# Performance work log

Hardware: AMD Instinct MI355X
Metric: run time of the kernel (lower is better)

Reference implementation:

```python
import jax, jax.numpy as jnp
import numpy as np

N_HEADS = 8
D_K = 64
NEG = 1e9


def setup_inputs() -> dict:
    key = jax.random.key(0)
    k1, k2, k3 = jax.random.split(key, 3)
    B, L, C = 4, 2048, 512
    x = jax.random.normal(k1, (B, L, C), dtype=jnp.float32)
    W_in = jax.random.normal(k2, (C, N_HEADS * D_K * 3), dtype=jnp.float32) * (C ** -0.5)
    b_in = jnp.zeros((N_HEADS * D_K * 3,), dtype=jnp.float32)
    W_out = jax.random.normal(k3, (N_HEADS * D_K, C), dtype=jnp.float32) * ((N_HEADS * D_K) ** -0.5)
    b_out = jnp.zeros((C,), dtype=jnp.float32)
    return {"x": x, "W_in": W_in, "b_in": b_in, "W_out": W_out, "b_out": b_out}


def reference(x, W_in, b_in, W_out, b_out):
    B, L, C = x.shape
    H, Dk = N_HEADS, D_K
    scale = Dk ** -0.5
    qkv = x @ W_in + b_in                       # [B, L, 3*H*Dk]
    qkv = qkv.reshape(B, L, H, 3 * Dk)
    q, k, v = jnp.split(qkv, 3, axis=-1)         # each [B, L, H, Dk]
    attn = jnp.einsum('bihd,bjhd->bijh', q, k) * scale  # [B, L, L, H]
    mask = jnp.tril(jnp.ones((L, L), dtype=x.dtype))[None, :, :, None]
    attn = attn * mask - NEG * (1.0 - mask)
    attn = jax.nn.softmax(attn, axis=2)          # softmax over j
    res = jnp.einsum('bijh,bjhd->bihd', attn, v)  # [B, L, H, Dk]
    res = res.reshape(B, L, H * Dk)
    res = res @ W_out + b_out
    return res + x
```

## Files before the change

### kernel.cpp

```cpp
#include <hip/hip_runtime.h>
#include <math.h>
#include <cstddef>


constexpr int B_SZ  = 4;
constexpr int L_SEQ = 2048;
constexpr int C_DIM = 512;
constexpr int H_N   = 8;
constexpr int DK    = 64;
constexpr int N_QKV = 1536;
constexpr int M_ROWS = B_SZ * L_SEQ;
constexpr float SCALE = 0.125f;
constexpr float DEFER_THR = 8.f;

typedef __attribute__((ext_vector_type(4))) float f32x4;
typedef __attribute__((ext_vector_type(8))) short bf16x8;

static __device__ inline ushort f2bf(float f) {
  unsigned u = __builtin_bit_cast(unsigned, f);
  u += 0x7fffu + ((u >> 16) & 1u);
  return (ushort)(u >> 16);
}

typedef __attribute__((address_space(1))) const unsigned int* gas1_t;
typedef __attribute__((address_space(3))) unsigned int* las3_t;
static __device__ inline void gload_lds16(const void* g, void* l) {
  __builtin_amdgcn_global_load_lds((gas1_t)g, (las3_t)l, 16, 0, 0);
}


__global__ __launch_bounds__(256) void convert_bf16(
    const float* __restrict__ src, ushort* __restrict__ dst, int n4) {
  const int i = blockIdx.x * 256 + threadIdx.x;
  if (i < n4) {
    const float4 v = reinterpret_cast<const float4*>(src)[i];
    ushort4 o;
    o.x = f2bf(v.x); o.y = f2bf(v.y); o.z = f2bf(v.z); o.w = f2bf(v.w);
    reinterpret_cast<ushort4*>(dst)[i] = o;
  }
}

__global__ __launch_bounds__(256) void transpose_bf16(
    const float* __restrict__ src, ushort* __restrict__ dst, int R, int C) {
  __shared__ ushort T[64][65];
  const int c0 = blockIdx.x * 64, r0 = blockIdx.y * 64;
#pragma unroll
  for (int p = 0; p < 16; ++p) {
    const int idx = threadIdx.x + p * 256;
    const int r = idx >> 6, c = idx & 63;
    T[r][c] = f2bf(src[(size_t)(r0 + r) * C + c0 + c]);
  }
  __syncthreads();
#pragma unroll
  for (int p = 0; p < 16; ++p) {
    const int idx = threadIdx.x + p * 256;
    const int r = idx >> 6, c = idx & 63;
    dst[(size_t)(c0 + r) * R + r0 + c] = T[c][r];
  }
}

template <int EPI>
__global__ __launch_bounds__(256) void gemm_bf16(
    const ushort* __restrict__ A, const ushort* __restrict__ Bt,
    const float* __restrict__ bias, ushort* __restrict__ Qo,
    ushort* __restrict__ Ko, ushort* __restrict__ Vto,
    float* __restrict__ outF, const float* __restrict__ resid,
    int N, int K) {
  __shared__ ushort Al[128 * 32];
  __shared__ ushort Bl[128 * 32];
  const int tid = threadIdx.x;
  const int w = tid >> 6, l = tid & 63;
  const int cc = l & 15, gg = l >> 4;
  const int bm = blockIdx.y * 128, bn = blockIdx.x * 128;
  const int wr = w >> 1, wc = w & 1;
  f32x4 acc[4][4] = {};

  for (int k0 = 0; k0 < K; k0 += 32) {
#pragma unroll
    for (int q = 0; q < 2; ++q) {
      const int cbase = q * 256 + w * 64;
      const int c = cbase + l;
      gload_lds16(A + (size_t)(bm + (c >> 2)) * K + k0 + (c & 3) * 8,
                  &Al[cbase * 8]);
      gload_lds16(Bt + (size_t)(bn + (c >> 2)) * K + k0 + (c & 3) * 8,
                  &Bl[cbase * 8]);
    }
    __syncthreads();
    bf16x8 aF[4], bF[4];
#pragma unroll
    for (int i = 0; i < 4; ++i)
      aF[i] = *reinterpret_cast<const bf16x8*>(
          &Al[(wr * 64 + i * 16 + cc) * 32 + gg * 8]);
#pragma unroll
    for (int j = 0; j < 4; ++j)
      bF[j] = *reinterpret_cast<const bf16x8*>(
          &Bl[(wc * 64 + j * 16 + cc) * 32 + gg * 8]);
#pragma unroll
    for (int i = 0; i < 4; ++i)
#pragma unroll
      for (int j = 0; j < 4; ++j)
        acc[i][j] = __builtin_amdgcn_mfma_f32_16x16x32_bf16(aF[i], bF[j],
                                                            acc[i][j], 0, 0, 0);
    __syncthreads();
  }

  if (EPI == 0) {
#pragma unroll
    for (int j = 0; j < 4; ++j) {
      const int colbase = bn + wc * 64 + j * 16;
      const int h = colbase / 192, rem = colbase % 192;
      const int type = rem / 64, d = (rem % 64) + cc;
      const float bv = bias[colbase + cc];
#pragma unroll
      for (int i = 0; i < 4; ++i) {
        const int rowbase = bm + wr * 64 + i * 16 + 4 * gg;
        const int b = rowbase >> 11, ll = rowbase & 2047;
        const size_t bh32 = (size_t)(b * H_N + h) * 32;
        if (type == 0) {
#pragma unroll
          for (int r = 0; r < 4; ++r)
            Qo[((size_t)(b * H_N + h) * L_SEQ + ll + r) * DK + d] =
                f2bf(acc[i][j][r] + bv);
        } else if (type == 1) {
#pragma unroll
          for (int r = 0; r < 4; ++r) {
            const int jg = ll + r;
            Ko[(bh32 + (jg >> 6)) * 4096 + (jg & 63) * 64 +
               (((d >> 3) ^ (jg & 7)) << 3) + (d & 7)] =
                f2bf(acc[i][j][r] + bv);
          }
        } else {
          ushort4 pk;
          pk.x = f2bf(acc[i][j][0] + bv);
          pk.y = f2bf(acc[i][j][1] + bv);
          pk.z = f2bf(acc[i][j][2] + bv);
          pk.w = f2bf(acc[i][j][3] + bv);
          const size_t idx = (bh32 + (ll >> 6)) * 4096 + (size_t)d * 64 +
                             ((((ll & 63) >> 3) ^ (d & 7)) << 3) + (ll & 7);
          *reinterpret_cast<ushort4*>(&Vto[idx]) = pk;
        }
      }
    }
  } else {
#pragma unroll
    for (int j = 0; j < 4; ++j) {
      const int col = bn + wc * 64 + j * 16 + cc;
      const float bv = bias[col];
#pragma unroll
      for (int i = 0; i < 4; ++i) {
        const int rowbase = bm + wr * 64 + i * 16 + 4 * gg;
#pragma unroll
        for (int r = 0; r < 4; ++r) {
          const size_t off = (size_t)(rowbase + r) * N + col;
          outF[off] = acc[i][j][r] + bv + resid[off];
        }
      }
    }
  }
}

#define STAGE(buf, tile)                                                     \
  {                                                                          \
    const ushort* kg_ = KoB + (size_t)(tile) * 4096 + w * 1024 + lane * 8;   \
    const ushort* vg_ = VtB + (size_t)(tile) * 4096 + w * 1024 + lane * 8;   \
    gload_lds16(kg_, &Ks[buf][w * 1024]);                                    \
    gload_lds16(kg_ + 512, &Ks[buf][w * 1024 + 512]);                        \
    gload_lds16(vg_, &Vs[buf][w * 1024]);                                    \
    gload_lds16(vg_ + 512, &Vs[buf][w * 1024 + 512]);                        \
  }

__global__ __launch_bounds__(256, 4) void attn_mfma(
    const ushort* __restrict__ Q, const ushort* __restrict__ Ko,
    const ushort* __restrict__ Vt, ushort* __restrict__ attn_out) {
  __shared__ ushort Ks[2][4096];
  __shared__ ushort Vs[2][4096];
  __shared__ ushort Pw_s[4][1024];
  const int id = blockIdx.x;
  const int bh = (id & 7) + 8 * ((id >> 3) & 3);
  const int qt = 31 - (id >> 5);
  const int tid = threadIdx.x;
  const int w = tid >> 6, lane = tid & 63;
  const int c = lane & 15, g = lane >> 4;
  const int b = bh >> 3, h = bh & 7;
  const ushort* KoB = Ko + (size_t)bh * 32 * 4096;
  const ushort* VtB = Vt + (size_t)bh * 32 * 4096;
  const int q0 = qt * 64 + w * 16;
  ushort* Pw = Pw_s[w];
  const int pc0 = (g ^ (c & 7)) * 8;
  const int pc1 = ((g + 4) ^ (c & 7)) * 8;

  bf16x8 qA[2];
  {
    const ushort* qp = Q + ((size_t)bh * L_SEQ + q0 + c) * DK + g * 8;
    qA[0] = *reinterpret_cast<const bf16x8*>(qp);
    qA[1] = *reinterpret_cast<const bf16x8*>(qp + 32);
  }

  f32x4 O[4] = {};
  float mrow[4] = {-INFINITY, -INFINITY, -INFINITY, -INFINITY};
  float lsum[4] = {};
  const f32x4 zero4 = {0.f, 0.f, 0.f, 0.f};

  STAGE(0, 0);
  __syncthreads();

  for (int jt = 0; jt <= qt; ++jt) {
    const int cur = jt & 1;
    if (jt < qt) STAGE(cur ^ 1, jt + 1);
    const ushort* Kc = Ks[cur];
    const ushort* Vc = Vs[cur];
    const int j0 = jt * 64;
    f32x4 S[4];
#pragma unroll
    for (int n = 0; n < 4; ++n) {
      const bf16x8 k0 = *reinterpret_cast<const bf16x8*>(&Kc[(n * 16 + c) * 64 + pc0]);
      const bf16x8 k1 = *reinterpret_cast<const bf16x8*>(&Kc[(n * 16 + c) * 64 + pc1]);
      S[n] = __builtin_amdgcn_mfma_f32_16x16x32_bf16(qA[0], k0, zero4, 0, 0, 0);
      S[n] = __builtin_amdgcn_mfma_f32_16x16x32_bf16(qA[1], k1, S[n], 0, 0, 0);
    }
    const bool diag = (jt == qt);
#pragma unroll
    for (int n = 0; n < 4; ++n)
#pragma unroll
      for (int r = 0; r < 4; ++r) {
        float v = S[n][r] * SCALE;
        if (diag && (j0 + n * 16 + c) > (q0 + 4 * g + r)) v = -INFINITY;
        S[n][r] = v;
      }
    float pm[4];
    int exceed = 0;
#pragma unroll
    for (int r = 0; r < 4; ++r) {
      pm[r] = fmaxf(fmaxf(S[0][r], S[1][r]), fmaxf(S[2][r], S[3][r]));
      exceed |= (pm[r] > mrow[r] + DEFER_THR);
    }
    if (__any(exceed)) {
#pragma unroll
      for (int r = 0; r < 4; ++r) {
        float fm = pm[r];
        fm = fmaxf(fm, __shfl_xor(fm, 1, 16));
        fm = fmaxf(fm, __shfl_xor(fm, 2, 16));
        fm = fmaxf(fm, __shfl_xor(fm, 4, 16));
        fm = fmaxf(fm, __shfl_xor(fm, 8, 16));
        const float mnew = fmaxf(mrow[r], fm);
        const float corr = __expf(mrow[r] - mnew);
        lsum[r] *= corr;
#pragma unroll
        for (int t = 0; t < 4; ++t) O[t][r] *= corr;
        mrow[r] = mnew;
      }
    }
#pragma unroll
    for (int n = 0; n < 4; ++n)
#pragma unroll
      for (int r = 0; r < 4; ++r) {
        const float p = __expf(S[n][r] - mrow[r]);
        S[n][r] = p;
        lsum[r] += p;
      }
#pragma unroll
    for (int n = 0; n < 4; ++n)
#pragma unroll
      for (int r = 0; r < 4; ++r) {
        const int row = 4 * g + r;
        Pw[row * 64 + ((2 * n + (c >> 3)) ^ (row & 7)) * 8 + (c & 7)] =
            f2bf(S[n][r]);
      }
    const bf16x8 pA0 = *reinterpret_cast<const bf16x8*>(&Pw[c * 64 + pc0]);
    const bf16x8 pA1 = *reinterpret_cast<const bf16x8*>(&Pw[c * 64 + pc1]);
#pragma unroll
    for (int t = 0; t < 4; ++t) {
      const bf16x8 v0 = *reinterpret_cast<const bf16x8*>(&Vc[(t * 16 + c) * 64 + pc0]);
      const bf16x8 v1 = *reinterpret_cast<const bf16x8*>(&Vc[(t * 16 + c) * 64 + pc1]);
      O[t] = __builtin_amdgcn_mfma_f32_16x16x32_bf16(pA0, v0, O[t], 0, 0, 0);
      O[t] = __builtin_amdgcn_mfma_f32_16x16x32_bf16(pA1, v1, O[t], 0, 0, 0);
    }
    __syncthreads();
  }
  float inv[4];
#pragma unroll
  for (int r = 0; r < 4; ++r) {
    float s = lsum[r];
    s += __shfl_xor(s, 1, 16);
    s += __shfl_xor(s, 2, 16);
    s += __shfl_xor(s, 4, 16);
    s += __shfl_xor(s, 8, 16);
    inv[r] = 1.f / s;
  }
#pragma unroll
  for (int t = 0; t < 4; ++t)
#pragma unroll
    for (int r = 0; r < 4; ++r)
      attn_out[((size_t)b * L_SEQ + q0 + 4 * g + r) * C_DIM + h * DK + t * 16 + c] =
          f2bf(O[t][r] * inv[r]);
}

extern "C" void kernel_launch(void* const* d_in, const int* in_sizes, int n_in,
                              void* d_out, int out_size, void* d_ws,
                              size_t ws_size, hipStream_t stream) {
  const float* x     = (const float*)d_in[0];
  const float* W_in  = (const float*)d_in[1];
  const float* b_in  = (const float*)d_in[2];
  const float* W_out = (const float*)d_in[3];
  const float* b_out = (const float*)d_in[4];
  float* out = (float*)d_out;

  ushort* xbf   = (ushort*)d_ws;
  ushort* WinT  = xbf + (size_t)M_ROWS * C_DIM;
  ushort* WoutT = WinT + (size_t)N_QKV * C_DIM;
  ushort* Qo    = WoutT + (size_t)C_DIM * C_DIM;
  ushort* Ko    = Qo + (size_t)M_ROWS * C_DIM;
  ushort* Vto   = Ko + (size_t)M_ROWS * C_DIM;
  ushort* attnb = Vto + (size_t)M_ROWS * C_DIM;

  convert_bf16<<<(M_ROWS * C_DIM / 4 + 255) / 256, 256, 0, stream>>>(
      x, xbf, M_ROWS * C_DIM / 4);
  transpose_bf16<<<dim3(N_QKV / 64, C_DIM / 64), 256, 0, stream>>>(
      W_in, WinT, C_DIM, N_QKV);
  transpose_bf16<<<dim3(C_DIM / 64, C_DIM / 64), 256, 0, stream>>>(
      W_out, WoutT, C_DIM, C_DIM);

  gemm_bf16<0><<<dim3(N_QKV / 128, M_ROWS / 128), 256, 0, stream>>>(
      xbf, WinT, b_in, Qo, Ko, Vto, nullptr, nullptr, N_QKV, C_DIM);
  attn_mfma<<<dim3(1024, 1, 1), 256, 0, stream>>>(Qo, Ko, Vto, attnb);
  gemm_bf16<1><<<dim3(C_DIM / 128, M_ROWS / 128), 256, 0, stream>>>(
      attnb, WoutT, b_out, nullptr, nullptr, nullptr, out, x, C_DIM, C_DIM);
}
```

Baseline: 98.33 us.

## Fold softmax scale into Q, use exp2, and pack P writes via permuted V layout

Q is pre-multiplied by scale*log2(e) in the QKV epilogue, so the attention loop no longer multiplies S by the scale and can use exp2 in place of exp. The defer threshold is rescaled to match. P is written to LDS as packed 8-byte bf16 vectors instead of 16 scalar stores, which requires permuting the key order within each 64-key tile. The V transpose layout is permuted the same way so the PV MFMA stays consistent. The cost is scalar, non-vectorized stores of V in the QKV epilogue.

```diff
diff --git a/kernel.cpp b/kernel.cpp
--- a/kernel.cpp
+++ b/kernel.cpp
@@ -1,6 +1,8 @@
 #include <hip/hip_runtime.h>
+#include <hip/hip_bf16.h>
 #include <math.h>
 #include <cstddef>
+#include <cstring>
 
 
 constexpr int B_SZ  = 4;
@@ -10,8 +12,8 @@
 constexpr int DK    = 64;
 constexpr int N_QKV = 1536;
 constexpr int M_ROWS = B_SZ * L_SEQ;
-constexpr float SCALE = 0.125f;
-constexpr float DEFER_THR = 8.f;
+constexpr float QSCALE = 0.125f * 1.44269504088896f;
+constexpr float DEFER_THR = 11.5f;
 
 typedef __attribute__((ext_vector_type(4))) float f32x4;
 typedef __attribute__((ext_vector_type(8))) short bf16x8;
@@ -20,6 +22,13 @@
   unsigned u = __builtin_bit_cast(unsigned, f);
   u += 0x7fffu + ((u >> 16) & 1u);
   return (ushort)(u >> 16);
+}
+
+static __device__ inline unsigned pack_bf2(float a, float b) {
+  const __hip_bfloat162 v = __float22bfloat162_rn(make_float2(a, b));
+  unsigned u;
+  __builtin_memcpy(&u, &v, 4);
+  return u;
 }
 
 typedef __attribute__((address_space(1))) const unsigned int* gas1_t;
@@ -120,7 +129,7 @@
 #pragma unroll
           for (int r = 0; r < 4; ++r)
             Qo[((size_t)(b * H_N + h) * L_SEQ + ll + r) * DK + d] =
-                f2bf(acc[i][j][r] + bv);
+                f2bf((acc[i][j][r] + bv) * QSCALE);
         } else if (type == 1) {
 #pragma unroll
           for (int r = 0; r < 4; ++r) {
@@ -130,14 +139,14 @@
                 f2bf(acc[i][j][r] + bv);
           }
         } else {
-          ushort4 pk;
-          pk.x = f2bf(acc[i][j][0] + bv);
-          pk.y = f2bf(acc[i][j][1] + bv);
-          pk.z = f2bf(acc[i][j][2] + bv);
-          pk.w = f2bf(acc[i][j][3] + bv);
-          const size_t idx = (bh32 + (ll >> 6)) * 4096 + (size_t)d * 64 +
-                             ((((ll & 63) >> 3) ^ (d & 7)) << 3) + (ll & 7);
-          *reinterpret_cast<ushort4*>(&Vto[idx]) = pk;
+#pragma unroll
+          for (int r = 0; r < 4; ++r) {
+            const int jj = (ll & 63) + r;
+            const int p = 4 * (jj & 15) + (jj >> 4);
+            const int phys = (((p >> 3) ^ (d & 7)) << 3) | (p & 7);
+            Vto[(bh32 + (ll >> 6)) * 4096 + (size_t)d * 64 + phys] =
+                f2bf(acc[i][j][r] + bv);
+          }
         }
       }
     }
@@ -218,15 +227,13 @@
       S[n] = __builtin_amdgcn_mfma_f32_16x16x32_bf16(qA[0], k0, zero4, 0, 0, 0);
       S[n] = __builtin_amdgcn_mfma_f32_16x16x32_bf16(qA[1], k1, S[n], 0, 0, 0);
     }
-    const bool diag = (jt == qt);
-#pragma unroll
-    for (int n = 0; n < 4; ++n)
-#pragma unroll
-      for (int r = 0; r < 4; ++r) {
-        float v = S[n][r] * SCALE;
-        if (diag && (j0 + n * 16 + c) > (q0 + 4 * g + r)) v = -INFINITY;
-        S[n][r] = v;
-      }
+    if (jt == qt) {
+#pragma unroll
+      for (int n = 0; n < 4; ++n)
+#pragma unroll
+        for (int r = 0; r < 4; ++r)
+          if ((j0 + n * 16 + c) > (q0 + 4 * g + r)) S[n][r] = -INFINITY;
+    }
     float pm[4];
     int exceed = 0;
 #pragma unroll
@@ -243,7 +250,7 @@
         fm = fmaxf(fm, __shfl_xor(fm, 4, 16));
         fm = fmaxf(fm, __shfl_xor(fm, 8, 16));
         const float mnew = fmaxf(mrow[r], fm);
-        const float corr = __expf(mrow[r] - mnew);
+        const float corr = __builtin_exp2f(mrow[r] - mnew);
         lsum[r] *= corr;
 #pragma unroll
         for (int t = 0; t < 4; ++t) O[t][r] *= corr;
@@ -254,18 +261,19 @@
     for (int n = 0; n < 4; ++n)
 #pragma unroll
       for (int r = 0; r < 4; ++r) {
-        const float p = __expf(S[n][r] - mrow[r]);
+        const float p = __builtin_exp2f(S[n][r] - mrow[r]);
         S[n][r] = p;
         lsum[r] += p;
       }
 #pragma unroll
-    for (int n = 0; n < 4; ++n)
-#pragma unroll
-      for (int r = 0; r < 4; ++r) {
-        const int row = 4 * g + r;
-        Pw[row * 64 + ((2 * n + (c >> 3)) ^ (row & 7)) * 8 + (c & 7)] =
-            f2bf(S[n][r]);
-      }
+    for (int r = 0; r < 4; ++r) {
+      const int row = 4 * g + r;
+      uint2 pk2;
+      pk2.x = pack_bf2(S[0][r], S[1][r]);
+      pk2.y = pack_bf2(S[2][r], S[3][r]);
+      *reinterpret_cast<uint2*>(
+          &Pw[row * 64 + (((c >> 1) ^ (row & 7)) << 3) + 4 * (c & 1)]) = pk2;
+    }
     const bf16x8 pA0 = *reinterpret_cast<const bf16x8*>(&Pw[c * 64 + pc0]);
     const bf16x8 pA1 = *reinterpret_cast<const bf16x8*>(&Pw[c * 64 + pc1]);
 #pragma unroll
```

Result: slower. 106.2 us (+8.1%).

## Software-pipeline QK^T one tile ahead and fold softmax scale into Q

Applied to the files above, without the earlier changes.

The attention loop now computes the QK^T MFMAs for the next key tile before doing softmax and PV on the current one. K and V are staged separately into ping-pong LDS buffers, so the matrix work can overlap the exponent and shuffle work. The softmax scale and log2(e) are folded into Q when the projection GEMM writes it out, and exp2 is used instead of expf, which drops a multiply per score. The deferral threshold is rescaled to match the base-2 domain. The cost is roughly doubled score registers (SA and SB), which could hurt occupancy, plus more complex staging and synchronisation logic.

```diff
diff --git a/kernel.cpp b/kernel.cpp
--- a/kernel.cpp
+++ b/kernel.cpp
@@ -1,4 +1,5 @@
 #include <hip/hip_runtime.h>
+#include <hip/hip_bf16.h>
 #include <math.h>
 #include <cstddef>
 
@@ -10,8 +11,8 @@
 constexpr int DK    = 64;
 constexpr int N_QKV = 1536;
 constexpr int M_ROWS = B_SZ * L_SEQ;
-constexpr float SCALE = 0.125f;
-constexpr float DEFER_THR = 8.f;
+constexpr float QSCALE = 0.125f * 1.44269504088896f;
+constexpr float DEFER_THR = 11.5f;
 
 typedef __attribute__((ext_vector_type(4))) float f32x4;
 typedef __attribute__((ext_vector_type(8))) short bf16x8;
@@ -120,7 +121,7 @@
 #pragma unroll
           for (int r = 0; r < 4; ++r)
             Qo[((size_t)(b * H_N + h) * L_SEQ + ll + r) * DK + d] =
-                f2bf(acc[i][j][r] + bv);
+                f2bf((acc[i][j][r] + bv) * QSCALE);
         } else if (type == 1) {
 #pragma unroll
           for (int r = 0; r < 4; ++r) {
@@ -159,12 +160,90 @@
   }
 }
 
-#define STAGE(buf, tile)                                                     \
+static __device__ __forceinline__ void qk_tile(
+    f32x4 (&S)[4], const ushort* __restrict__ Kc, const bf16x8 (&qA)[2],
+    int c, int pc0, int pc1) {
+  const f32x4 zero4 = {0.f, 0.f, 0.f, 0.f};
+#pragma unroll
+  for (int n = 0; n < 4; ++n) {
+    const bf16x8 k0 = *reinterpret_cast<const bf16x8*>(&Kc[(n * 16 + c) * 64 + pc0]);
+    const bf16x8 k1 = *reinterpret_cast<const bf16x8*>(&Kc[(n * 16 + c) * 64 + pc1]);
+    S[n] = __builtin_amdgcn_mfma_f32_16x16x32_bf16(qA[0], k0, zero4, 0, 0, 0);
+    S[n] = __builtin_amdgcn_mfma_f32_16x16x32_bf16(qA[1], k1, S[n], 0, 0, 0);
+  }
+}
+
+static __device__ __forceinline__ void finish_tile(
+    f32x4 (&S)[4], f32x4 (&O)[4], float (&mrow)[4], float (&lsum)[4],
+    const ushort* __restrict__ Vc, ushort* __restrict__ Pw,
+    int jt, int qt, int q0, int c, int g, int pc0, int pc1) {
+  if (jt == qt) {
+    const int j0 = jt * 64;
+#pragma unroll
+    for (int n = 0; n < 4; ++n)
+#pragma unroll
+      for (int r = 0; r < 4; ++r)
+        if ((j0 + n * 16 + c) > (q0 + 4 * g + r)) S[n][r] = -INFINITY;
+  }
+  float pm[4];
+  int exceed = 0;
+#pragma unroll
+  for (int r = 0; r < 4; ++r) {
+    pm[r] = fmaxf(fmaxf(S[0][r], S[1][r]), fmaxf(S[2][r], S[3][r]));
+    exceed |= (pm[r] > mrow[r] + DEFER_THR);
+  }
+  if (__any(exceed)) {
+#pragma unroll
+    for (int r = 0; r < 4; ++r) {
+      float fm = pm[r];
+      fm = fmaxf(fm, __shfl_xor(fm, 1, 16));
+      fm = fmaxf(fm, __shfl_xor(fm, 2, 16));
+      fm = fmaxf(fm, __shfl_xor(fm, 4, 16));
+      fm = fmaxf(fm, __shfl_xor(fm, 8, 16));
+      const float mnew = fmaxf(mrow[r], fm);
+      const float corr = __builtin_exp2f(mrow[r] - mnew);
+      lsum[r] *= corr;
+#pragma unroll
+      for (int t = 0; t < 4; ++t) O[t][r] *= corr;
+      mrow[r] = mnew;
+    }
+  }
+#pragma unroll
+  for (int n = 0; n < 4; ++n)
+#pragma unroll
+    for (int r = 0; r < 4; ++r) {
+      const float p = __builtin_exp2f(S[n][r] - mrow[r]);
+      S[n][r] = p;
+      lsum[r] += p;
+    }
+#pragma unroll
+  for (int n = 0; n < 4; ++n)
+#pragma unroll
+    for (int r = 0; r < 4; ++r) {
+      const int row = 4 * g + r;
+      Pw[row * 64 + ((2 * n + (c >> 3)) ^ (row & 7)) * 8 + (c & 7)] =
+          f2bf(S[n][r]);
+    }
+  const bf16x8 pA0 = *reinterpret_cast<const bf16x8*>(&Pw[c * 64 + pc0]);
+  const bf16x8 pA1 = *reinterpret_cast<const bf16x8*>(&Pw[c * 64 + pc1]);
+#pragma unroll
+  for (int t = 0; t < 4; ++t) {
+    const bf16x8 v0 = *reinterpret_cast<const bf16x8*>(&Vc[(t * 16 + c) * 64 + pc0]);
+    const bf16x8 v1 = *reinterpret_cast<const bf16x8*>(&Vc[(t * 16 + c) * 64 + pc1]);
+    O[t] = __builtin_amdgcn_mfma_f32_16x16x32_bf16(pA0, v0, O[t], 0, 0, 0);
+    O[t] = __builtin_amdgcn_mfma_f32_16x16x32_bf16(pA1, v1, O[t], 0, 0, 0);
+  }
+}
+
+#define STAGE_K(buf, tile)                                                   \
   {                                                                          \
     const ushort* kg_ = KoB + (size_t)(tile) * 4096 + w * 1024 + lane * 8;   \
-    const ushort* vg_ = VtB + (size_t)(tile) * 4096 + w * 1024 + lane * 8;   \
     gload_lds16(kg_, &Ks[buf][w * 1024]);                                    \
     gload_lds16(kg_ + 512, &Ks[buf][w * 1024 + 512]);                        \
+  }
+#define STAGE_V(buf, tile)                                                   \
+  {                                                                          \
+    const ushort* vg_ = VtB + (size_t)(tile) * 4096 + w * 1024 + lane * 8;   \
     gload_lds16(vg_, &Vs[buf][w * 1024]);                                    \
     gload_lds16(vg_ + 512, &Vs[buf][w * 1024 + 512]);                        \
   }
@@ -199,83 +278,37 @@
   f32x4 O[4] = {};
   float mrow[4] = {-INFINITY, -INFINITY, -INFINITY, -INFINITY};
   float lsum[4] = {};
-  const f32x4 zero4 = {0.f, 0.f, 0.f, 0.f};
-
-  STAGE(0, 0);
+  f32x4 SA[4], SB[4];
+
+  STAGE_K(0, 0);
+  STAGE_V(0, 0);
+  if (qt >= 1) STAGE_K(1, 1);
   __syncthreads();
-
-  for (int jt = 0; jt <= qt; ++jt) {
-    const int cur = jt & 1;
-    if (jt < qt) STAGE(cur ^ 1, jt + 1);
-    const ushort* Kc = Ks[cur];
-    const ushort* Vc = Vs[cur];
-    const int j0 = jt * 64;
-    f32x4 S[4];
-#pragma unroll
-    for (int n = 0; n < 4; ++n) {
-      const bf16x8 k0 = *reinterpret_cast<const bf16x8*>(&Kc[(n * 16 + c) * 64 + pc0]);
-      const bf16x8 k1 = *reinterpret_cast<const bf16x8*>(&Kc[(n * 16 + c) * 64 + pc1]);
-      S[n] = __builtin_amdgcn_mfma_f32_16x16x32_bf16(qA[0], k0, zero4, 0, 0, 0);
-      S[n] = __builtin_amdgcn_mfma_f32_16x16x32_bf16(qA[1], k1, S[n], 0, 0, 0);
-    }
-    const bool diag = (jt == qt);
-#pragma unroll
-    for (int n = 0; n < 4; ++n)
-#pragma unroll
-      for (int r = 0; r < 4; ++r) {
-        float v = S[n][r] * SCALE;
-        if (diag && (j0 + n * 16 + c) > (q0 + 4 * g + r)) v = -INFINITY;
-        S[n][r] = v;
+  qk_tile(SA, Ks[0], qA, c, pc0, pc1);
+  __syncthreads();
+
+  int jt = 0;
+  while (true) {
+    {
+      if (jt + 1 <= qt) {
+        qk_tile(SB, Ks[1], qA, c, pc0, pc1);
+        STAGE_V(1, jt + 1);
       }
-    float pm[4];
-    int exceed = 0;
-#pragma unroll
-    for (int r = 0; r < 4; ++r) {
-      pm[r] = fmaxf(fmaxf(S[0][r], S[1][r]), fmaxf(S[2][r], S[3][r]));
-      exceed |= (pm[r] > mrow[r] + DEFER_THR);
-    }
-    if (__any(exceed)) {
-#pragma unroll
-      for (int r = 0; r < 4; ++r) {
-        float fm = pm[r];
-        fm = fmaxf(fm, __shfl_xor(fm, 1, 16));
-        fm = fmaxf(fm, __shfl_xor(fm, 2, 16));
-        fm = fmaxf(fm, __shfl_xor(fm, 4, 16));
-        fm = fmaxf(fm, __shfl_xor(fm, 8, 16));
-        const float mnew = fmaxf(mrow[r], fm);
-        const float corr = __expf(mrow[r] - mnew);
-        lsum[r] *= corr;
-#pragma unroll
-        for (int t = 0; t < 4; ++t) O[t][r] *= corr;
-        mrow[r] = mnew;
+      if (jt + 2 <= qt) STAGE_K(0, jt + 2);
+      finish_tile(SA, O, mrow, lsum, Vs[0], Pw, jt, qt, q0, c, g, pc0, pc1);
+      __syncthreads();
+      if (++jt > qt) break;
+    }
+    {
+      if (jt + 1 <= qt) {
+        qk_tile(SA, Ks[0], qA, c, pc0, pc1);
+        STAGE_V(0, jt + 1);
       }
-    }
-#pragma unroll
-    for (int n = 0; n < 4; ++n)
-#pragma unroll
-      for (int r = 0; r < 4; ++r) {
-        const float p = __expf(S[n][r] - mrow[r]);
-        S[n][r] = p;
-        lsum[r] += p;
-      }
-#pragma unroll
-    for (int n = 0; n < 4; ++n)
-#pragma unroll
-      for (int r = 0; r < 4; ++r) {
-        const int row = 4 * g + r;
-        Pw[row * 64 + ((2 * n + (c >> 3)) ^ (row & 7)) * 8 + (c & 7)] =
-            f2bf(S[n][r]);
-      }
-    const bf16x8 pA0 = *reinterpret_cast<const bf16x8*>(&Pw[c * 64 + pc0]);
-    const bf16x8 pA1 = *reinterpret_cast<const bf16x8*>(&Pw[c * 64 + pc1]);
-#pragma unroll
-    for (int t = 0; t < 4; ++t) {
-      const bf16x8 v0 = *reinterpret_cast<const bf16x8*>(&Vc[(t * 16 + c) * 64 + pc0]);
-      const bf16x8 v1 = *reinterpret_cast<const bf16x8*>(&Vc[(t * 16 + c) * 64 + pc1]);
-      O[t] = __builtin_amdgcn_mfma_f32_16x16x32_bf16(pA0, v0, O[t], 0, 0, 0);
-      O[t] = __builtin_amdgcn_mfma_f32_16x16x32_bf16(pA1, v1, O[t], 0, 0, 0);
-    }
-    __syncthreads();
+      if (jt + 2 <= qt) STAGE_K(1, jt + 2);
+      finish_tile(SB, O, mrow, lsum, Vs[1], Pw, jt, qt, q0, c, g, pc0, pc1);
+      __syncthreads();
+      if (++jt > qt) break;
+    }
   }
   float inv[4];
 #pragma unroll
```

New measurement: 101.8 us. 1.04x slower.
